# Kernel optimization log

Measured on AMD Instinct MI355X. Metric: run time of the kernel, lower is better.

Reference implementation:

```python
import jax, jax.numpy as jnp
import numpy as np

TRUNC = (24, 24, 24)
OUT = (32, 32, 32)


def setup_inputs() -> dict:
    key = jax.random.key(0)
    x = jax.random.normal(key, (8, 32, 48, 48, 48), dtype=jnp.float32)
    return {"x": x}


def reference(x):
    # "DCT" as implemented in the source: real part of an ortho-normalized 3D FFT
    x_dct = jnp.real(jnp.fft.fftn(x, axes=(2, 3, 4), norm='ortho'))
    # crop to low-frequency corner, zero-pad up to output_size
    x_crop = x_dct[:, :, :TRUNC[0], :TRUNC[1], :TRUNC[2]]
    pad = ((0, 0), (0, 0),
           (0, OUT[0] - TRUNC[0]),
           (0, OUT[1] - TRUNC[1]),
           (0, OUT[2] - TRUNC[2]))
    x_pad = jnp.pad(x_crop, pad)
    # inverse transform on the output_size grid, keep real part
    x_idct = jnp.real(jnp.fft.ifftn(x_pad, axes=(2, 3, 4), norm='ortho'))
    return x_idct
```

## Files before the change

### kernel.cpp

```cpp
#include <hip/hip_runtime.h>
#include <math.h>


#define TWO_PI_48 0.13089969389957470f
#define TWO_PI_32 0.19634954084936207f
#define NORM_F    1.6611664e-05f

typedef _Float16 half8  __attribute__((ext_vector_type(8)));
typedef _Float16 half4v __attribute__((ext_vector_type(4)));
typedef float    f32x4  __attribute__((ext_vector_type(4)));

__device__ _Float16 T1frag[2][3][2][64][8];
__device__ _Float16 T2frag[2][3][2][64][8];
__device__ __align__(16) _Float16 TK2frag[2][4][3][64][8];
__device__ __align__(16) _Float16 MB2frag[2][4][2][64][8];
__device__ __align__(16) _Float16 TB3frag[2][2][2][64][8];

__device__ int g_twdone = 0;

__global__ void k_init_tw() {
  if (g_twdone) return;
  const int idx = blockIdx.x * 256 + threadIdx.x;
  if (idx < 3072) {
    const int j  = idx & 7;
    const int l  = (idx >> 3) & 63;
    const int ks = (idx >> 9) & 1;
    const int t  = idx >> 10;
    const int k  = ks * 32 + (l >> 4) * 8 + j;
    {
      const int m = t * 16 + (l & 15);
      float v = 0.f;
      if (k < 48) {
        const float a = (float)(((m % 24) * k) % 48) * TWO_PI_48;
        v = (m < 24) ? cosf(a) : -sinf(a);
      }
      const _Float16 h = (_Float16)v;
      T1frag[0][t][ks][l][j] = h;
      T1frag[1][t][ks][l][j] = (_Float16)(v - (float)h);
    }
    {
      const int c = t * 16 + (l & 15);
      float v = 0.f;
      if (k < 48) {
        const float a = (float)(((c % 24) * k) % 48) * TWO_PI_48;
        v = (c < 24) ? cosf(a) : sinf(a);
      }
      const _Float16 h = (_Float16)v;
      T2frag[0][t][ks][l][j] = h;
      T2frag[1][t][ks][l][j] = (_Float16)(v - (float)h);
    }
  } else if (idx < 3072 + 6144) {
    const int local = idx - 3072;
    const int j = local & 7, l = (local >> 3) & 63;
    const int rest = local >> 9;
    const int ks = rest % 3, mt = rest / 3;
    const int m   = mt * 16 + (l & 15);
    const int kap = ks * 32 + (l >> 4) * 8 + j;
    const int n1  = kap % 48;
    const bool isVi = kap >= 48;
    const int m1  = m & 31;
    const bool isWi = m >= 32;
    float acc = 0.f;
    for (int k1 = 0; k1 < 24; ++k1) {
      float s32v, c32v, s48v, c48v;
      sincosf((float)((k1 * m1) % 32) * TWO_PI_32, &s32v, &c32v);
      sincosf((float)((k1 * n1) % 48) * TWO_PI_48, &s48v, &c48v);
      acc = fmaf(isWi ? s32v : c32v, isVi ? s48v : c48v, acc);
    }
    const _Float16 h = (_Float16)acc;
    TK2frag[0][mt][ks][l][j] = h;
    TK2frag[1][mt][ks][l][j] = (_Float16)(acc - (float)h);
  } else if (idx < 3072 + 6144 + 4096) {
    const int local = idx - (3072 + 6144);
    const int j = local & 7, l = (local >> 3) & 63;
    const int rest = local >> 9;
    const int ks = rest & 1, mt = rest >> 1;
    const int m   = mt * 16 + (l & 15);
    const int kap = ks * 32 + (l >> 4) * 8 + j;
    float v = 0.f;
    if (kap < 48) {
      const int k2 = kap % 24;
      const int m2 = m & 31;
      float s, c;
      sincosf((float)((k2 * m2) % 32) * TWO_PI_32, &s, &c);
      if (m < 32) v = (kap < 24) ? c : -s;
      else        v = (kap < 24) ? s :  c;
    }
    const _Float16 h = (_Float16)v;
    MB2frag[0][mt][ks][l][j] = h;
    MB2frag[1][mt][ks][l][j] = (_Float16)(v - (float)h);
  } else if (idx < 15360) {
    const int local = idx - (3072 + 6144 + 4096);
    const int j = local & 7, l = (local >> 3) & 63;
    const int rest = local >> 9;
    const int ks = rest & 1, nt = rest >> 1;
    const int m3  = nt * 16 + (l & 15);
    const int kap = ks * 32 + (l >> 4) * 8 + j;
    float v = 0.f;
    if (kap < 48) {
      const int k3 = kap % 24;
      float s, c;
      sincosf((float)((k3 * m3) % 32) * TWO_PI_32, &s, &c);
      v = (kap < 24) ? c : -s;
    }
    const _Float16 h = (_Float16)v;
    TB3frag[0][nt][ks][l][j] = h;
    TB3frag[1][nt][ks][l][j] = (_Float16)(v - (float)h);
  }
}

__device__ inline void split8(const float* qf, half8& h, half8& lo) {
#pragma unroll
  for (int j = 0; j < 8; ++j) {
    const _Float16 hh = (_Float16)qf[j];
    h[j]  = hh;
    lo[j] = (_Float16)(qf[j] - (float)hh);
  }
}

__global__ __launch_bounds__(64, 3) void k1_waveslab(const float* __restrict__ x,
                                                     float2* __restrict__ V) {
  const int n1   = blockIdx.x;
  const int bc   = blockIdx.y;
  const int lane = threadIdx.x;

  __shared__ __align__(16) unsigned char arena[13824];
  _Float16* Uh = (_Float16*)arena;
  _Float16* Ul = (_Float16*)(arena + 6912);
  float*    D2 = (float*)arena;

  const int c16  = lane & 15;
  const int kgrp = lane >> 4;
  const int kb   = kgrp * 8;

  half8 t1h[3][2], t1l[3][2], t2h[3][2], t2l[3][2];
#pragma unroll
  for (int mt = 0; mt < 3; ++mt)
#pragma unroll
    for (int ks = 0; ks < 2; ++ks) {
      t1h[mt][ks] = *(const half8*)&T1frag[0][mt][ks][lane][0];
      t1l[mt][ks] = *(const half8*)&T1frag[1][mt][ks][lane][0];
      t2h[mt][ks] = *(const half8*)&T2frag[0][mt][ks][lane][0];
      t2l[mt][ks] = *(const half8*)&T2frag[1][mt][ks][lane][0];
    }

#pragma unroll
  for (int p = 0; p < 3; ++p) {
    const int i = lane + 64 * p;
    const int which = i / 48, r = i % 48;
    _Float16* base = (which & 2) ? Ul : Uh;
    *(half8*)&base[r * 72 + 48 + (which & 1) * 8] = (half8){};
  }

  const float* xs = x + (size_t)(bc * 48 + n1) * 2304;

  float4 fa0, fb0, fa1, fb1;
  {
    const float4* p0 = (const float4*)(xs + c16 * 48 + kb);
    fa0 = p0[0]; fb0 = p0[1];
    const int k1i = 32 + kb;
    if (k1i < 48) {
      const float4* p1 = (const float4*)(xs + c16 * 48 + k1i);
      fa1 = p1[0]; fb1 = p1[1];
    } else { fa1 = make_float4(0.f,0.f,0.f,0.f); fb1 = fa1; }
  }

#pragma unroll
  for (int nt = 0; nt < 3; ++nt) {
    float4 na0, nb0, na1, nb1;
    if (nt < 2) {
      const int c = (nt + 1) * 16 + c16;
      const float4* p0 = (const float4*)(xs + c * 48 + kb);
      na0 = p0[0]; nb0 = p0[1];
      const int k1i = 32 + kb;
      if (k1i < 48) {
        const float4* p1 = (const float4*)(xs + c * 48 + k1i);
        na1 = p1[0]; nb1 = p1[1];
      } else { na1 = make_float4(0.f,0.f,0.f,0.f); nb1 = na1; }
    }

    f32x4 acc0 = {}, acc1 = {}, acc2 = {};
#pragma unroll
    for (int ks = 0; ks < 2; ++ks) {
      const float4 qa = ks ? fa1 : fa0;
      const float4 qb = ks ? fb1 : fb0;
      const float qf[8] = {qa.x, qa.y, qa.z, qa.w, qb.x, qb.y, qb.z, qb.w};
      half8 bh, bl;
      split8(qf, bh, bl);
#pragma unroll
      for (int mt = 0; mt < 3; ++mt) {
        f32x4& acc = (mt == 0) ? acc0 : (mt == 1) ? acc1 : acc2;
        acc = __builtin_amdgcn_mfma_f32_16x16x32_f16(t1h[mt][ks], bh, acc, 0, 0, 0);
        acc = __builtin_amdgcn_mfma_f32_16x16x32_f16(t1h[mt][ks], bl, acc, 0, 0, 0);
        acc = __builtin_amdgcn_mfma_f32_16x16x32_f16(t1l[mt][ks], bh, acc, 0, 0, 0);
      }
    }

    {
      const int cc = nt * 16 + c16;
#pragma unroll
      for (int mt = 0; mt < 3; ++mt) {
        const int r0 = mt * 16 + kgrp * 4;
        const f32x4 acc = (mt == 0) ? acc0 : (mt == 1) ? acc1 : acc2;
#pragma unroll
        for (int r = 0; r < 4; ++r) {
          const float v = acc[r];
          const _Float16 h = (_Float16)v;
          Uh[(r0 + r) * 72 + cc] = h;
          Ul[(r0 + r) * 72 + cc] = (_Float16)(v - (float)h);
        }
      }
    }

    fa0 = na0; fb0 = nb0; fa1 = na1; fb1 = nb1;
  }

  f32x4 a2[3][3] = {};
#pragma unroll
  for (int ks = 0; ks < 2; ++ks) {
#pragma unroll
    for (int mt = 0; mt < 3; ++mt) {
      const half8 ah = *(const half8*)&Uh[(mt * 16 + c16) * 72 + ks * 32 + kb];
      const half8 al = *(const half8*)&Ul[(mt * 16 + c16) * 72 + ks * 32 + kb];
#pragma unroll
      for (int nt2 = 0; nt2 < 3; ++nt2) {
        a2[mt][nt2] = __builtin_amdgcn_mfma_f32_16x16x32_f16(ah, t2h[nt2][ks], a2[mt][nt2], 0, 0, 0);
        a2[mt][nt2] = __builtin_amdgcn_mfma_f32_16x16x32_f16(ah, t2l[nt2][ks], a2[mt][nt2], 0, 0, 0);
        a2[mt][nt2] = __builtin_amdgcn_mfma_f32_16x16x32_f16(al, t2h[nt2][ks], a2[mt][nt2], 0, 0, 0);
      }
    }
  }

#pragma unroll
  for (int mt = 0; mt < 3; ++mt)
#pragma unroll
    for (int nt2 = 0; nt2 < 3; ++nt2) {
      const int r0 = mt * 16 + kgrp * 4;
      const int cc = nt2 * 16 + c16;
#pragma unroll
      for (int r = 0; r < 4; ++r)
        D2[(r0 + r) * 68 + cc] = a2[mt][nt2][r];
    }

#pragma unroll
  for (int q = 0; q < 9; ++q) {
    const int idx = lane + 64 * q;
    const int k3 = idx / 24, k2 = idx % 24;
    const float grr = D2[k3 * 68 + k2];
    const float gis = D2[(k3 + 24) * 68 + k2 + 24];
    const float gir = D2[(k3 + 24) * 68 + k2];
    const float grs = D2[k3 * 68 + k2 + 24];
    V[(size_t)bc * 27648 + (size_t)k3 * 1152 + n1 * 24 + k2] =
        make_float2(grr + gis, gir - grs);
  }
}

__global__ __launch_bounds__(192) void k2_mfma(const float2* __restrict__ V,
                                               float2* __restrict__ W) {
  const int k3   = blockIdx.x;
  const int byy  = blockIdx.y;
  const int tid  = threadIdx.x;
  const int lane = tid & 63;
  const int w    = tid >> 6;

  __shared__ __align__(16) float Bb[48 * 100];

  half8 kth[4][3], ktl[4][3];
#pragma unroll
  for (int mt = 0; mt < 4; ++mt)
#pragma unroll
    for (int ks = 0; ks < 3; ++ks) {
      kth[mt][ks] = *(const half8*)&TK2frag[0][mt][ks][lane][0];
      ktl[mt][ks] = *(const half8*)&TK2frag[1][mt][ks][lane][0];
    }

  const int kbase = (lane >> 4) * 8;
  const int c16   = lane & 15;
  const int cc    = w * 16 + c16;
  const int sE    = cc / 24, k2E = cc % 24;
  const int rbase = (lane >> 4) * 4;

  float4 vr[6];
  {
    const float4* g0 = (const float4*)(V + ((size_t)((byy * 4 + 0) * 24 + k3)) * 1152);
    const float4* g1 = (const float4*)(V + ((size_t)((byy * 4 + 1) * 24 + k3)) * 1152);
#pragma unroll
    for (int jj = 0; jj < 6; ++jj)
      vr[jj] = (jj < 3 ? g0 : g1)[tid + 192 * (jj % 3)];
  }

  for (int g = 0; g < 2; ++g) {
    const int bcp = byy * 2 + g;

    if (g) __syncthreads();

#pragma unroll
    for (int jj = 0; jj < 6; ++jj) {
      const int s = jj / 3;
      const int r = tid + 192 * (jj % 3);
      const int n1 = r / 12, c4 = r % 12;
      const float4 f = vr[jj];
      float* bp = &Bb[(s * 24 + c4 * 2) * 100 + n1];
      bp[0]   = f.x;  bp[48]  = f.y;
      bp[100] = f.z;  bp[148] = f.w;
    }
    if (g < 1) {
      const float4* g0 = (const float4*)(V + ((size_t)((bcp * 2 + 2) * 24 + k3)) * 1152);
      const float4* g1 = (const float4*)(V + ((size_t)((bcp * 2 + 3) * 24 + k3)) * 1152);
#pragma unroll
      for (int jj = 0; jj < 6; ++jj)
        vr[jj] = (jj < 3 ? g0 : g1)[tid + 192 * (jj % 3)];
    }
    __syncthreads();

    f32x4 a0 = {}, a1 = {}, a2 = {}, a3 = {};
#pragma unroll
    for (int ks = 0; ks < 3; ++ks) {
      const float4 q0 = *(const float4*)&Bb[cc * 100 + ks * 32 + kbase];
      const float4 q1 = *(const float4*)&Bb[cc * 100 + ks * 32 + kbase + 4];
      const float qf[8] = {q0.x, q0.y, q0.z, q0.w, q1.x, q1.y, q1.z, q1.w};
      half8 bh, bl;
      split8(qf, bh, bl);
#pragma unroll
      for (int mt = 0; mt < 4; ++mt) {
        f32x4& acc = (mt == 0) ? a0 : (mt == 1) ? a1 : (mt == 2) ? a2 : a3;
        acc = __builtin_amdgcn_mfma_f32_16x16x32_f16(kth[mt][ks], bh, acc, 0, 0, 0);
        acc = __builtin_amdgcn_mfma_f32_16x16x32_f16(kth[mt][ks], bl, acc, 0, 0, 0);
        acc = __builtin_amdgcn_mfma_f32_16x16x32_f16(ktl[mt][ks], bh, acc, 0, 0, 0);
      }
    }

    const int bc = bcp * 2 + sE;
    float2* wp = W + (size_t)bc * 18432 + (size_t)k3 * 24 + k2E;
#pragma unroll
    for (int mt = 0; mt < 2; ++mt) {
      const f32x4 wr = (mt == 0) ? a0 : a1;
      const f32x4 wi = (mt == 0) ? a2 : a3;
#pragma unroll
      for (int r = 0; r < 4; ++r) {
        const int m1 = mt * 16 + rbase + r;
        wp[(size_t)m1 * 576] = make_float2(wr[r], wi[r]);
      }
    }
  }
}

__global__ __launch_bounds__(128) void k3_mfma(const float2* __restrict__ W,
                                               float* __restrict__ out) {
  const int m1   = blockIdx.x;
  const int byy  = blockIdx.y;
  const int tid  = threadIdx.x;
  const int lane = tid & 63;
  const int w    = tid >> 6;

  __shared__ __align__(16) float Bt[32 * 68];
  __shared__ __align__(16) float Zb[32 * 68];

  half8 mbh[4][2], mbl[4][2];
#pragma unroll
  for (int mt = 0; mt < 4; ++mt)
#pragma unroll
    for (int ks = 0; ks < 2; ++ks) {
      mbh[mt][ks] = *(const half8*)&MB2frag[0][mt][ks][lane][0];
      mbl[mt][ks] = *(const half8*)&MB2frag[1][mt][ks][lane][0];
    }
  half8 tb3h[2], tb3l[2];
#pragma unroll
  for (int ks = 0; ks < 2; ++ks) {
    tb3h[ks] = *(const half8*)&TB3frag[0][w][ks][lane][0];
    tb3l[ks] = *(const half8*)&TB3frag[1][w][ks][lane][0];
  }

  for (int i = tid; i < 8 * 68; i += 128)  Bt[(24 + i / 68) * 68 + (i % 68)] = 0.f;
  for (int i = tid; i < 24 * 20; i += 128) Bt[(i / 20) * 68 + 48 + (i % 20)] = 0.f;
  for (int i = tid; i < 32 * 20; i += 128) Zb[(i / 20) * 68 + 48 + (i % 20)] = 0.f;

  const int kbase = (lane >> 4) * 8;
  const int c16   = lane & 15;
  const int cc    = w * 16 + c16;
  const int rbase = (lane >> 4) * 4;

  float4 vr0, vr1, vr2;
  {
    const float4* g4 = (const float4*)(W + (size_t)(byy * 2) * 18432 + (size_t)m1 * 576);
    vr0 = g4[tid];
    vr1 = g4[tid + 128];
    if (tid < 32) vr2 = g4[tid + 256];
  }

  for (int g = 0; g < 2; ++g) {
    const int bc = byy * 2 + g;

    {
      const float4 fr[3] = {vr0, vr1, vr2};
#pragma unroll
      for (int jj = 0; jj < 3; ++jj) {
        const int i4 = tid + 128 * jj;
        if (jj < 2 || tid < 32) {
          const int k3 = i4 / 12, c4 = i4 % 12;
          const float4 f = fr[jj];
          Bt[k3 * 68 + 2 * c4]          = f.x;
          Bt[k3 * 68 + 24 + 2 * c4]     = f.y;
          Bt[k3 * 68 + 2 * c4 + 1]      = f.z;
          Bt[k3 * 68 + 24 + 2 * c4 + 1] = f.w;
        }
      }
    }
    if (g < 1) {
      const float4* g4 = (const float4*)(W + (size_t)(bc + 1) * 18432 + (size_t)m1 * 576);
      vr0 = g4[tid];
      vr1 = g4[tid + 128];
      if (tid < 32) vr2 = g4[tid + 256];
    }
    __syncthreads();

    f32x4 z0 = {}, z1 = {}, z2 = {}, z3 = {};
#pragma unroll
    for (int ks = 0; ks < 2; ++ks) {
      const float4 q0 = *(const float4*)&Bt[cc * 68 + ks * 32 + kbase];
      const float4 q1 = *(const float4*)&Bt[cc * 68 + ks * 32 + kbase + 4];
      const float qf[8] = {q0.x, q0.y, q0.z, q0.w, q1.x, q1.y, q1.z, q1.w};
      half8 bh, bl;
      split8(qf, bh, bl);
#pragma unroll
      for (int mt = 0; mt < 4; ++mt) {
        f32x4& acc = (mt == 0) ? z0 : (mt == 1) ? z1 : (mt == 2) ? z2 : z3;
        acc = __builtin_amdgcn_mfma_f32_16x16x32_f16(mbh[mt][ks], bh, acc, 0, 0, 0);
        acc = __builtin_amdgcn_mfma_f32_16x16x32_f16(mbh[mt][ks], bl, acc, 0, 0, 0);
        acc = __builtin_amdgcn_mfma_f32_16x16x32_f16(mbl[mt][ks], bh, acc, 0, 0, 0);
      }
    }
    if (cc < 24) {
#pragma unroll
      for (int mt = 0; mt < 4; ++mt) {
        const f32x4 acc = (mt == 0) ? z0 : (mt == 1) ? z1 : (mt == 2) ? z2 : z3;
        const int row0 = mt * 16 + rbase;
#pragma unroll
        for (int r = 0; r < 4; ++r) {
          const int row = row0 + r;
          if (row < 32) Zb[row * 68 + cc]              = acc[r];
          else          Zb[(row - 32) * 68 + 24 + cc]  = acc[r];
        }
      }
    }
    __syncthreads();

    f32x4 o0 = {}, o1 = {};
#pragma unroll
    for (int ks = 0; ks < 2; ++ks) {
#pragma unroll
      for (int mt = 0; mt < 2; ++mt) {
        const float4 q0 = *(const float4*)&Zb[(mt * 16 + c16) * 68 + ks * 32 + kbase];
        const float4 q1 = *(const float4*)&Zb[(mt * 16 + c16) * 68 + ks * 32 + kbase + 4];
        const float qf[8] = {q0.x, q0.y, q0.z, q0.w, q1.x, q1.y, q1.z, q1.w};
        half8 ah, al;
        split8(qf, ah, al);
        f32x4& acc = (mt == 0) ? o0 : o1;
        acc = __builtin_amdgcn_mfma_f32_16x16x32_f16(ah, tb3h[ks], acc, 0, 0, 0);
        acc = __builtin_amdgcn_mfma_f32_16x16x32_f16(ah, tb3l[ks], acc, 0, 0, 0);
        acc = __builtin_amdgcn_mfma_f32_16x16x32_f16(al, tb3h[ks], acc, 0, 0, 0);
      }
    }
    float* op = out + (size_t)(bc * 32 + m1) * 1024;
#pragma unroll
    for (int mt = 0; mt < 2; ++mt) {
      const f32x4 acc = (mt == 0) ? o0 : o1;
#pragma unroll
      for (int r = 0; r < 4; ++r) {
        const int m2 = mt * 16 + rbase + r;
        op[m2 * 32 + cc] = acc[r] * NORM_F;
      }
    }
  }

  if (tid == 0 && blockIdx.x == 0 && blockIdx.y == 0) g_twdone = 1;
}

extern "C" void kernel_launch(void* const* d_in, const int* in_sizes, int n_in,
                              void* d_out, int out_size, void* d_ws, size_t ws_size,
                              hipStream_t stream) {
  const float* x = (const float*)d_in[0];
  float* out = (float*)d_out;
  float2* V = (float2*)d_ws;
  float2* W = (float2*)((char*)d_ws + 56623104);

  k_init_tw   <<<dim3(60), dim3(256), 0, stream>>>();
  k1_waveslab <<<dim3(48, 256), dim3(64), 0, stream>>>(x, V);
  k2_mfma     <<<dim3(24, 64), dim3(192), 0, stream>>>(V, W);
  k3_mfma     <<<dim3(32, 128), dim3(128), 0, stream>>>(W, out);
}
```

Measured before the change: 79.21 us.

## Remove per-block batch loops in k2/k3 and store k1 intermediate as fp32

k2 and k3 each used to process two batch slices per block, with register prefetch of the next slice. Each block now handles one slice and the grid is doubled, trading that overlap for more parallelism and lower per-block latency. In k1, the intermediate is now stored in shared memory as fp32 and split into fp16 hi/lo just before the second MFMA stage, instead of being stored pre-split. This makes the store side cheaper at the cost of extra conversion work at load time, with the same total shared memory footprint.

```diff
diff --git a/kernel.cpp b/kernel.cpp
--- a/kernel.cpp
+++ b/kernel.cpp
@@ -124,10 +124,8 @@
   const int bc   = blockIdx.y;
   const int lane = threadIdx.x;
 
-  __shared__ __align__(16) unsigned char arena[13824];
-  _Float16* Uh = (_Float16*)arena;
-  _Float16* Ul = (_Float16*)(arena + 6912);
-  float*    D2 = (float*)arena;
+  __shared__ __align__(16) float U[48 * 68];
+  float* D2 = U;
 
   const int c16  = lane & 15;
   const int kgrp = lane >> 4;
@@ -146,10 +144,9 @@
 
 #pragma unroll
   for (int p = 0; p < 3; ++p) {
-    const int i = lane + 64 * p;
-    const int which = i / 48, r = i % 48;
-    _Float16* base = (which & 2) ? Ul : Uh;
-    *(half8*)&base[r * 72 + 48 + (which & 1) * 8] = (half8){};
+    const int fl = lane + 64 * p;
+    const int row = fl >> 2, c4 = fl & 3;
+    *(f32x4*)&U[row * 68 + 48 + c4 * 4] = (f32x4){};
   }
 
   const float* xs = x + (size_t)(bc * 48 + n1) * 2304;
@@ -203,12 +200,8 @@
         const int r0 = mt * 16 + kgrp * 4;
         const f32x4 acc = (mt == 0) ? acc0 : (mt == 1) ? acc1 : acc2;
 #pragma unroll
-        for (int r = 0; r < 4; ++r) {
-          const float v = acc[r];
-          const _Float16 h = (_Float16)v;
-          Uh[(r0 + r) * 72 + cc] = h;
-          Ul[(r0 + r) * 72 + cc] = (_Float16)(v - (float)h);
-        }
+        for (int r = 0; r < 4; ++r)
+          U[(r0 + r) * 68 + cc] = acc[r];
       }
     }
 
@@ -220,8 +213,11 @@
   for (int ks = 0; ks < 2; ++ks) {
 #pragma unroll
     for (int mt = 0; mt < 3; ++mt) {
-      const half8 ah = *(const half8*)&Uh[(mt * 16 + c16) * 72 + ks * 32 + kb];
-      const half8 al = *(const half8*)&Ul[(mt * 16 + c16) * 72 + ks * 32 + kb];
+      const float4 q0 = *(const float4*)&U[(mt * 16 + c16) * 68 + ks * 32 + kb];
+      const float4 q1 = *(const float4*)&U[(mt * 16 + c16) * 68 + ks * 32 + kb + 4];
+      const float qf[8] = {q0.x, q0.y, q0.z, q0.w, q1.x, q1.y, q1.z, q1.w};
+      half8 ah, al;
+      split8(qf, ah, al);
 #pragma unroll
       for (int nt2 = 0; nt2 < 3; ++nt2) {
         a2[mt][nt2] = __builtin_amdgcn_mfma_f32_16x16x32_f16(ah, t2h[nt2][ks], a2[mt][nt2], 0, 0, 0);
@@ -258,7 +254,7 @@
 __global__ __launch_bounds__(192) void k2_mfma(const float2* __restrict__ V,
                                                float2* __restrict__ W) {
   const int k3   = blockIdx.x;
-  const int byy  = blockIdx.y;
+  const int bcp  = blockIdx.y;
   const int tid  = threadIdx.x;
   const int lane = tid & 63;
   const int w    = tid >> 6;
@@ -282,65 +278,52 @@
 
   float4 vr[6];
   {
-    const float4* g0 = (const float4*)(V + ((size_t)((byy * 4 + 0) * 24 + k3)) * 1152);
-    const float4* g1 = (const float4*)(V + ((size_t)((byy * 4 + 1) * 24 + k3)) * 1152);
+    const float4* g0 = (const float4*)(V + ((size_t)((bcp * 2 + 0) * 24 + k3)) * 1152);
+    const float4* g1 = (const float4*)(V + ((size_t)((bcp * 2 + 1) * 24 + k3)) * 1152);
 #pragma unroll
     for (int jj = 0; jj < 6; ++jj)
       vr[jj] = (jj < 3 ? g0 : g1)[tid + 192 * (jj % 3)];
   }
 
-  for (int g = 0; g < 2; ++g) {
-    const int bcp = byy * 2 + g;
-
-    if (g) __syncthreads();
-
-#pragma unroll
-    for (int jj = 0; jj < 6; ++jj) {
-      const int s = jj / 3;
-      const int r = tid + 192 * (jj % 3);
-      const int n1 = r / 12, c4 = r % 12;
-      const float4 f = vr[jj];
-      float* bp = &Bb[(s * 24 + c4 * 2) * 100 + n1];
-      bp[0]   = f.x;  bp[48]  = f.y;
-      bp[100] = f.z;  bp[148] = f.w;
-    }
-    if (g < 1) {
-      const float4* g0 = (const float4*)(V + ((size_t)((bcp * 2 + 2) * 24 + k3)) * 1152);
-      const float4* g1 = (const float4*)(V + ((size_t)((bcp * 2 + 3) * 24 + k3)) * 1152);
-#pragma unroll
-      for (int jj = 0; jj < 6; ++jj)
-        vr[jj] = (jj < 3 ? g0 : g1)[tid + 192 * (jj % 3)];
-    }
-    __syncthreads();
-
-    f32x4 a0 = {}, a1 = {}, a2 = {}, a3 = {};
-#pragma unroll
-    for (int ks = 0; ks < 3; ++ks) {
-      const float4 q0 = *(const float4*)&Bb[cc * 100 + ks * 32 + kbase];
-      const float4 q1 = *(const float4*)&Bb[cc * 100 + ks * 32 + kbase + 4];
-      const float qf[8] = {q0.x, q0.y, q0.z, q0.w, q1.x, q1.y, q1.z, q1.w};
-      half8 bh, bl;
-      split8(qf, bh, bl);
-#pragma unroll
-      for (int mt = 0; mt < 4; ++mt) {
-        f32x4& acc = (mt == 0) ? a0 : (mt == 1) ? a1 : (mt == 2) ? a2 : a3;
-        acc = __builtin_amdgcn_mfma_f32_16x16x32_f16(kth[mt][ks], bh, acc, 0, 0, 0);
-        acc = __builtin_amdgcn_mfma_f32_16x16x32_f16(kth[mt][ks], bl, acc, 0, 0, 0);
-        acc = __builtin_amdgcn_mfma_f32_16x16x32_f16(ktl[mt][ks], bh, acc, 0, 0, 0);
-      }
-    }
-
-    const int bc = bcp * 2 + sE;
-    float2* wp = W + (size_t)bc * 18432 + (size_t)k3 * 24 + k2E;
-#pragma unroll
-    for (int mt = 0; mt < 2; ++mt) {
-      const f32x4 wr = (mt == 0) ? a0 : a1;
-      const f32x4 wi = (mt == 0) ? a2 : a3;
-#pragma unroll
-      for (int r = 0; r < 4; ++r) {
-        const int m1 = mt * 16 + rbase + r;
-        wp[(size_t)m1 * 576] = make_float2(wr[r], wi[r]);
-      }
+#pragma unroll
+  for (int jj = 0; jj < 6; ++jj) {
+    const int s = jj / 3;
+    const int r = tid + 192 * (jj % 3);
+    const int n1 = r / 12, c4 = r % 12;
+    const float4 f = vr[jj];
+    float* bp = &Bb[(s * 24 + c4 * 2) * 100 + n1];
+    bp[0]   = f.x;  bp[48]  = f.y;
+    bp[100] = f.z;  bp[148] = f.w;
+  }
+  __syncthreads();
+
+  f32x4 a0 = {}, a1 = {}, a2 = {}, a3 = {};
+#pragma unroll
+  for (int ks = 0; ks < 3; ++ks) {
+    const float4 q0 = *(const float4*)&Bb[cc * 100 + ks * 32 + kbase];
+    const float4 q1 = *(const float4*)&Bb[cc * 100 + ks * 32 + kbase + 4];
+    const float qf[8] = {q0.x, q0.y, q0.z, q0.w, q1.x, q1.y, q1.z, q1.w};
+    half8 bh, bl;
+    split8(qf, bh, bl);
+#pragma unroll
+    for (int mt = 0; mt < 4; ++mt) {
+      f32x4& acc = (mt == 0) ? a0 : (mt == 1) ? a1 : (mt == 2) ? a2 : a3;
+      acc = __builtin_amdgcn_mfma_f32_16x16x32_f16(kth[mt][ks], bh, acc, 0, 0, 0);
+      acc = __builtin_amdgcn_mfma_f32_16x16x32_f16(kth[mt][ks], bl, acc, 0, 0, 0);
+      acc = __builtin_amdgcn_mfma_f32_16x16x32_f16(ktl[mt][ks], bh, acc, 0, 0, 0);
+    }
+  }
+
+  const int bc = bcp * 2 + sE;
+  float2* wp = W + (size_t)bc * 18432 + (size_t)k3 * 24 + k2E;
+#pragma unroll
+  for (int mt = 0; mt < 2; ++mt) {
+    const f32x4 wr = (mt == 0) ? a0 : a1;
+    const f32x4 wi = (mt == 0) ? a2 : a3;
+#pragma unroll
+    for (int r = 0; r < 4; ++r) {
+      const int m1 = mt * 16 + rbase + r;
+      wp[(size_t)m1 * 576] = make_float2(wr[r], wi[r]);
     }
   }
 }
@@ -348,7 +331,7 @@
 __global__ __launch_bounds__(128) void k3_mfma(const float2* __restrict__ W,
                                                float* __restrict__ out) {
   const int m1   = blockIdx.x;
-  const int byy  = blockIdx.y;
+  const int bc   = blockIdx.y;
   const int tid  = threadIdx.x;
   const int lane = tid & 63;
   const int w    = tid >> 6;
@@ -382,94 +365,84 @@
 
   float4 vr0, vr1, vr2;
   {
-    const float4* g4 = (const float4*)(W + (size_t)(byy * 2) * 18432 + (size_t)m1 * 576);
+    const float4* g4 = (const float4*)(W + (size_t)bc * 18432 + (size_t)m1 * 576);
     vr0 = g4[tid];
     vr1 = g4[tid + 128];
     if (tid < 32) vr2 = g4[tid + 256];
   }
 
-  for (int g = 0; g < 2; ++g) {
-    const int bc = byy * 2 + g;
-
-    {
-      const float4 fr[3] = {vr0, vr1, vr2};
-#pragma unroll
-      for (int jj = 0; jj < 3; ++jj) {
-        const int i4 = tid + 128 * jj;
-        if (jj < 2 || tid < 32) {
-          const int k3 = i4 / 12, c4 = i4 % 12;
-          const float4 f = fr[jj];
-          Bt[k3 * 68 + 2 * c4]          = f.x;
-          Bt[k3 * 68 + 24 + 2 * c4]     = f.y;
-          Bt[k3 * 68 + 2 * c4 + 1]      = f.z;
-          Bt[k3 * 68 + 24 + 2 * c4 + 1] = f.w;
-        }
-      }
-    }
-    if (g < 1) {
-      const float4* g4 = (const float4*)(W + (size_t)(bc + 1) * 18432 + (size_t)m1 * 576);
-      vr0 = g4[tid];
-      vr1 = g4[tid + 128];
-      if (tid < 32) vr2 = g4[tid + 256];
-    }
-    __syncthreads();
-
-    f32x4 z0 = {}, z1 = {}, z2 = {}, z3 = {};
-#pragma unroll
-    for (int ks = 0; ks < 2; ++ks) {
-      const float4 q0 = *(const float4*)&Bt[cc * 68 + ks * 32 + kbase];
-      const float4 q1 = *(const float4*)&Bt[cc * 68 + ks * 32 + kbase + 4];
+  {
+    const float4 fr[3] = {vr0, vr1, vr2};
+#pragma unroll
+    for (int jj = 0; jj < 3; ++jj) {
+      const int i4 = tid + 128 * jj;
+      if (jj < 2 || tid < 32) {
+        const int k3 = i4 / 12, c4 = i4 % 12;
+        const float4 f = fr[jj];
+        Bt[k3 * 68 + 2 * c4]          = f.x;
+        Bt[k3 * 68 + 24 + 2 * c4]     = f.y;
+        Bt[k3 * 68 + 2 * c4 + 1]      = f.z;
+        Bt[k3 * 68 + 24 + 2 * c4 + 1] = f.w;
+      }
+    }
+  }
+  __syncthreads();
+
+  f32x4 z0 = {}, z1 = {}, z2 = {}, z3 = {};
+#pragma unroll
+  for (int ks = 0; ks < 2; ++ks) {
+    const float4 q0 = *(const float4*)&Bt[cc * 68 + ks * 32 + kbase];
+    const float4 q1 = *(const float4*)&Bt[cc * 68 + ks * 32 + kbase + 4];
+    const float qf[8] = {q0.x, q0.y, q0.z, q0.w, q1.x, q1.y, q1.z, q1.w};
+    half8 bh, bl;
+    split8(qf, bh, bl);
+#pragma unroll
+    for (int mt = 0; mt < 4; ++mt) {
+      f32x4& acc = (mt == 0) ? z0 : (mt == 1) ? z1 : (mt == 2) ? z2 : z3;
+      acc = __builtin_amdgcn_mfma_f32_16x16x32_f16(mbh[mt][ks], bh, acc, 0, 0, 0);
+      acc = __builtin_amdgcn_mfma_f32_16x16x32_f16(mbh[mt][ks], bl, acc, 0, 0, 0);
+      acc = __builtin_amdgcn_mfma_f32_16x16x32_f16(mbl[mt][ks], bh, acc, 0, 0, 0);
+    }
+  }
+  if (cc < 24) {
+#pragma unroll
+    for (int mt = 0; mt < 4; ++mt) {
+      const f32x4 acc = (mt == 0) ? z0 : (mt == 1) ? z1 : (mt == 2) ? z2 : z3;
+      const int row0 = mt * 16 + rbase;
+#pragma unroll
+      for (int r = 0; r < 4; ++r) {
+        const int row = row0 + r;
+        if (row < 32) Zb[row * 68 + cc]              = acc[r];
+        else          Zb[(row - 32) * 68 + 24 + cc]  = acc[r];
+      }
+    }
+  }
+  __syncthreads();
+
+  f32x4 o0 = {}, o1 = {};
+#pragma unroll
+  for (int ks = 0; ks < 2; ++ks) {
+#pragma unroll
+    for (int mt = 0; mt < 2; ++mt) {
+      const float4 q0 = *(const float4*)&Zb[(mt * 16 + c16) * 68 + ks * 32 + kbase];
+      const float4 q1 = *(const float4*)&Zb[(mt * 16 + c16) * 68 + ks * 32 + kbase + 4];
       const float qf[8] = {q0.x, q0.y, q0.z, q0.w, q1.x, q1.y, q1.z, q1.w};
-      half8 bh, bl;
-      split8(qf, bh, bl);
-#pragma unroll
-      for (int mt = 0; mt < 4; ++mt) {
-        f32x4& acc = (mt == 0) ? z0 : (mt == 1) ? z1 : (mt == 2) ? z2 : z3;
-        acc = __builtin_amdgcn_mfma_f32_16x16x32_f16(mbh[mt][ks], bh, acc, 0, 0, 0);
-        acc = __builtin_amdgcn_mfma_f32_16x16x32_f16(mbh[mt][ks], bl, acc, 0, 0, 0);
-        acc = __builtin_amdgcn_mfma_f32_16x16x32_f16(mbl[mt][ks], bh, acc, 0, 0, 0);
-      }
-    }
-    if (cc < 24) {
-#pragma unroll
-      for (int mt = 0; mt < 4; ++mt) {
-        const f32x4 acc = (mt == 0) ? z0 : (mt == 1) ? z1 : (mt == 2) ? z2 : z3;
-        const int row0 = mt * 16 + rbase;
-#pragma unroll
-        for (int r = 0; r < 4; ++r) {
-          const int row = row0 + r;
-          if (row < 32) Zb[row * 68 + cc]              = acc[r];
-          else          Zb[(row - 32) * 68 + 24 + cc]  = acc[r];
-        }
-      }
-    }
-    __syncthreads();
-
-    f32x4 o0 = {}, o1 = {};
-#pragma unroll
-    for (int ks = 0; ks < 2; ++ks) {
-#pragma unroll
-      for (int mt = 0; mt < 2; ++mt) {
-        const float4 q0 = *(const float4*)&Zb[(mt * 16 + c16) * 68 + ks * 32 + kbase];
-        const float4 q1 = *(const float4*)&Zb[(mt * 16 + c16) * 68 + ks * 32 + kbase + 4];
-        const float qf[8] = {q0.x, q0.y, q0.z, q0.w, q1.x, q1.y, q1.z, q1.w};
-        half8 ah, al;
-        split8(qf, ah, al);
-        f32x4& acc = (mt == 0) ? o0 : o1;
-        acc = __builtin_amdgcn_mfma_f32_16x16x32_f16(ah, tb3h[ks], acc, 0, 0, 0);
-        acc = __builtin_amdgcn_mfma_f32_16x16x32_f16(ah, tb3l[ks], acc, 0, 0, 0);
-        acc = __builtin_amdgcn_mfma_f32_16x16x32_f16(al, tb3h[ks], acc, 0, 0, 0);
-      }
-    }
-    float* op = out + (size_t)(bc * 32 + m1) * 1024;
-#pragma unroll
-    for (int mt = 0; mt < 2; ++mt) {
-      const f32x4 acc = (mt == 0) ? o0 : o1;
-#pragma unroll
-      for (int r = 0; r < 4; ++r) {
-        const int m2 = mt * 16 + rbase + r;
-        op[m2 * 32 + cc] = acc[r] * NORM_F;
-      }
+      half8 ah, al;
+      split8(qf, ah, al);
+      f32x4& acc = (mt == 0) ? o0 : o1;
+      acc = __builtin_amdgcn_mfma_f32_16x16x32_f16(ah, tb3h[ks], acc, 0, 0, 0);
+      acc = __builtin_amdgcn_mfma_f32_16x16x32_f16(ah, tb3l[ks], acc, 0, 0, 0);
+      acc = __builtin_amdgcn_mfma_f32_16x16x32_f16(al, tb3h[ks], acc, 0, 0, 0);
+    }
+  }
+  float* op = out + (size_t)(bc * 32 + m1) * 1024;
+#pragma unroll
+  for (int mt = 0; mt < 2; ++mt) {
+    const f32x4 acc = (mt == 0) ? o0 : o1;
+#pragma unroll
+    for (int r = 0; r < 4; ++r) {
+      const int m2 = mt * 16 + rbase + r;
+      op[m2 * 32 + cc] = acc[r] * NORM_F;
     }
   }
 
@@ -486,6 +459,6 @@
 
   k_init_tw   <<<dim3(60), dim3(256), 0, stream>>>();
   k1_waveslab <<<dim3(48, 256), dim3(64), 0, stream>>>(x, V);
-  k2_mfma     <<<dim3(24, 64), dim3(192), 0, stream>>>(V, W);
-  k3_mfma     <<<dim3(32, 128), dim3(128), 0, stream>>>(W, out);
-}
+  k2_mfma     <<<dim3(24, 128), dim3(192), 0, stream>>>(V, W);
+  k3_mfma     <<<dim3(32, 256), dim3(128), 0, stream>>>(W, out);
+}
```

Measured after the change: 80.59 us. Within noise of the previous version (+1.7%).

## Pack four waves per k1 block and stage intermediate as fp32 in LDS

Applied to the files above, without the earlier changes.

k1 now runs four independent wave-slabs per 256-thread block instead of one wave per block, with each wave owning its own LDS region. The intermediate U is stored once as fp32 and split into hi/lo fp16 halves at read time, instead of storing separate hi and lo fp16 arrays. This cuts launch granularity and halves the number of LDS stores in the first stage, at the cost of more LDS per block (about 52KB), which may limit how many blocks fit per CU, plus extra conversion work after the load.

```diff
diff --git a/kernel.cpp b/kernel.cpp
--- a/kernel.cpp
+++ b/kernel.cpp
@@ -118,16 +118,17 @@
   }
 }
 
-__global__ __launch_bounds__(64, 3) void k1_waveslab(const float* __restrict__ x,
-                                                     float2* __restrict__ V) {
-  const int n1   = blockIdx.x;
+__global__ __launch_bounds__(256, 3) void k1_waveslab(const float* __restrict__ x,
+                                                      float2* __restrict__ V) {
+  const int bx   = blockIdx.x;
   const int bc   = blockIdx.y;
-  const int lane = threadIdx.x;
-
-  __shared__ __align__(16) unsigned char arena[13824];
-  _Float16* Uh = (_Float16*)arena;
-  _Float16* Ul = (_Float16*)(arena + 6912);
-  float*    D2 = (float*)arena;
+  const int wv   = threadIdx.x >> 6;
+  const int lane = threadIdx.x & 63;
+  const int n1   = bx * 4 + wv;
+
+  __shared__ __align__(16) float pool[4 * 48 * 68];
+  float* U  = pool + wv * (48 * 68);
+  float* D2 = U;
 
   const int c16  = lane & 15;
   const int kgrp = lane >> 4;
@@ -146,10 +147,9 @@
 
 #pragma unroll
   for (int p = 0; p < 3; ++p) {
-    const int i = lane + 64 * p;
-    const int which = i / 48, r = i % 48;
-    _Float16* base = (which & 2) ? Ul : Uh;
-    *(half8*)&base[r * 72 + 48 + (which & 1) * 8] = (half8){};
+    const int fl = lane + 64 * p;
+    const int row = fl >> 2, c4 = fl & 3;
+    *(f32x4*)&U[row * 68 + 48 + c4 * 4] = (f32x4){};
   }
 
   const float* xs = x + (size_t)(bc * 48 + n1) * 2304;
@@ -203,12 +203,8 @@
         const int r0 = mt * 16 + kgrp * 4;
         const f32x4 acc = (mt == 0) ? acc0 : (mt == 1) ? acc1 : acc2;
 #pragma unroll
-        for (int r = 0; r < 4; ++r) {
-          const float v = acc[r];
-          const _Float16 h = (_Float16)v;
-          Uh[(r0 + r) * 72 + cc] = h;
-          Ul[(r0 + r) * 72 + cc] = (_Float16)(v - (float)h);
-        }
+        for (int r = 0; r < 4; ++r)
+          U[(r0 + r) * 68 + cc] = acc[r];
       }
     }
 
@@ -220,8 +216,11 @@
   for (int ks = 0; ks < 2; ++ks) {
 #pragma unroll
     for (int mt = 0; mt < 3; ++mt) {
-      const half8 ah = *(const half8*)&Uh[(mt * 16 + c16) * 72 + ks * 32 + kb];
-      const half8 al = *(const half8*)&Ul[(mt * 16 + c16) * 72 + ks * 32 + kb];
+      const float4 q0 = *(const float4*)&U[(mt * 16 + c16) * 68 + ks * 32 + kb];
+      const float4 q1 = *(const float4*)&U[(mt * 16 + c16) * 68 + ks * 32 + kb + 4];
+      const float qf[8] = {q0.x, q0.y, q0.z, q0.w, q1.x, q1.y, q1.z, q1.w};
+      half8 ah, al;
+      split8(qf, ah, al);
 #pragma unroll
       for (int nt2 = 0; nt2 < 3; ++nt2) {
         a2[mt][nt2] = __builtin_amdgcn_mfma_f32_16x16x32_f16(ah, t2h[nt2][ks], a2[mt][nt2], 0, 0, 0);
@@ -485,7 +484,7 @@
   float2* W = (float2*)((char*)d_ws + 56623104);
 
   k_init_tw   <<<dim3(60), dim3(256), 0, stream>>>();
-  k1_waveslab <<<dim3(48, 256), dim3(64), 0, stream>>>(x, V);
+  k1_waveslab <<<dim3(12, 256), dim3(256), 0, stream>>>(x, V);
   k2_mfma     <<<dim3(24, 64), dim3(192), 0, stream>>>(V, W);
   k3_mfma     <<<dim3(32, 128), dim3(128), 0, stream>>>(W, out);
 }
```

After: 78.17 us (median of 2 runs). About the same (-1.3%).
